# Performance work log

Hardware: AMD Instinct MI355X
Metric: run time of the kernel (lower is better)

The kernel has to match this reference:

```python
import jax, jax.numpy as jnp
import numpy as np

D_MODEL = 2048
NUM_HEADS = 16
HEAD_DIM = D_MODEL // NUM_HEADS
SCALE = 1.0 / np.sqrt(HEAD_DIM).astype(np.float32)
NEG_INF = -1e9


def setup_inputs() -> dict:
    key = jax.random.key(0)
    ks = jax.random.split(key, 10)
    B, S = 2, 2048
    x = jax.random.normal(ks[0], (B, S, D_MODEL), dtype=jnp.float32)
    # causal lower-triangular mask, broadcastable over (B, H)
    causal_mask = jnp.tril(jnp.ones((S, S), dtype=jnp.int32))[None, None]
    init = 1.0 / np.sqrt(D_MODEL)
    def lin(kw, kb):
        W = jax.random.uniform(kw, (D_MODEL, D_MODEL), jnp.float32, -init, init)
        b = jax.random.uniform(kb, (D_MODEL,), jnp.float32, -init, init)
        return W, b
    Wq, bq = lin(ks[1], ks[2])
    Wk, bk = lin(ks[3], ks[4])
    Wv, bv = lin(ks[5], ks[6])
    Wo, bo = lin(ks[7], ks[8])
    return {"x": x, "causal_mask": causal_mask,
            "Wq": Wq, "bq": bq, "Wk": Wk, "bk": bk,
            "Wv": Wv, "bv": bv, "Wo": Wo, "bo": bo}


def reference(x, causal_mask, Wq, bq, Wk, bk, Wv, bv, Wo, bo):
    B, S, _ = x.shape
    def proj(W, b):
        # torch Linear: x @ W.T + b -> (B, H, S, Dh)
        y = jnp.einsum('bsd,ed->bse', x, W) + b
        return y.reshape(B, S, NUM_HEADS, HEAD_DIM).transpose(0, 2, 1, 3)
    q = proj(Wq, bq)
    k = proj(Wk, bk)
    v = proj(Wv, bv)
    # apply_rope is a no-op stub in the source; q, k unchanged.
    scores = jnp.einsum('bhqd,bhkd->bhqk', q, k) * SCALE
    scores = jnp.where(causal_mask == 0, NEG_INF, scores)
    attn = jax.nn.softmax(scores, axis=-1)
    out = jnp.einsum('bhqk,bhkd->bhqd', attn, v)
    out = out.transpose(0, 2, 1, 3).reshape(B, S, D_MODEL)
    return jnp.einsum('bsd,ed->bse', out, Wo) + bo
```

## Files before the change

kernel.cpp:

```cpp
#include <hip/hip_runtime.h>
#include <hip/hip_bf16.h>
#include <stdint.h>
#include <stddef.h>

typedef __bf16 bf16_t;
typedef __bf16 bf16x4_t __attribute__((ext_vector_type(4)));
typedef __bf16 bf16x8_t __attribute__((ext_vector_type(8)));
typedef float f32x4 __attribute__((ext_vector_type(4)));

#define D_MODEL 2048
#define NHEADS 16
#define HDIM 128
#define SEQ 2048
#define BATCH 2
#define MTOT (BATCH * SEQ)
#define SCALE_F 0.08838834764831845f

#define AS1 __attribute__((address_space(1)))
#define AS3 __attribute__((address_space(3)))

__device__ __forceinline__ void load_lds16(const bf16_t* g, bf16_t* l) {
  __builtin_amdgcn_global_load_lds((AS1 void*)(g), (AS3 void*)(l), 16, 0, 0);
}

__global__ void cast_kernel(const float* __restrict__ src, bf16_t* __restrict__ dst, int n4) {
  int i = blockIdx.x * blockDim.x + threadIdx.x;
  if (i < n4) {
    float4 v = ((const float4*)src)[i];
    bf16x4_t o;
    o.x = (bf16_t)v.x; o.y = (bf16_t)v.y; o.z = (bf16_t)v.z; o.w = (bf16_t)v.w;
    ((bf16x4_t*)dst)[i] = o;
  }
}

__global__ __launch_bounds__(256) void gemm_fused(
    const bf16_t* __restrict__ A, const bf16_t* __restrict__ Bm, int mode,
    const float* __restrict__ bias0, const float* __restrict__ bias1,
    const float* __restrict__ bias2,
    bf16_t* __restrict__ Qo, bf16_t* __restrict__ Ko, bf16_t* __restrict__ Vto,
    float* __restrict__ Out) {
  const int K = 2048;
  __shared__ __align__(16) bf16_t lA[128 * 32];
  __shared__ __align__(16) bf16_t lB[128 * 32];
  const int m0 = blockIdx.x * 128;
  const int n0 = blockIdx.y * 128;
  const int t = threadIdx.x;
  const int w = t >> 6, lane = t & 63;
  const int wm = w & 1, wn = w >> 1;
  const int la = lane & 15, lb = lane >> 4;

  f32x4 acc[4][4];
  f32x4 zero = {0.f, 0.f, 0.f, 0.f};
#pragma unroll
  for (int i = 0; i < 4; i++)
#pragma unroll
    for (int j = 0; j < 4; j++) acc[i][j] = zero;

  const bf16_t* gA0 = A + (size_t)(m0 + (t >> 2)) * K + (t & 3) * 8;
  const bf16_t* gA1 = gA0 + (size_t)64 * K;
  const bf16_t* gB0 = Bm + (size_t)(n0 + (t >> 2)) * K + (t & 3) * 8;
  const bf16_t* gB1 = gB0 + (size_t)64 * K;
  bf16_t* sA = lA + t * 8;
  bf16_t* sB = lB + t * 8;

  for (int k0 = 0; k0 < K; k0 += 32) {
    __syncthreads();
    load_lds16(gA0 + k0, sA);
    load_lds16(gA1 + k0, sA + 2048);
    load_lds16(gB0 + k0, sB);
    load_lds16(gB1 + k0, sB + 2048);
    __syncthreads();
    bf16x8_t af[4], bfr[4];
#pragma unroll
    for (int mt = 0; mt < 4; mt++)
      af[mt] = *(const bf16x8_t*)(lA + (wm * 64 + mt * 16 + la) * 32 + lb * 8);
#pragma unroll
    for (int nt = 0; nt < 4; nt++)
      bfr[nt] = *(const bf16x8_t*)(lB + (wn * 64 + nt * 16 + la) * 32 + lb * 8);
#pragma unroll
    for (int mt = 0; mt < 4; mt++)
#pragma unroll
      for (int nt = 0; nt < 4; nt++)
        acc[mt][nt] = __builtin_amdgcn_mfma_f32_16x16x32_bf16(af[mt], bfr[nt], acc[mt][nt], 0, 0, 0);
  }

  if (mode == 0) {
#pragma unroll
    for (int mt = 0; mt < 4; mt++) {
#pragma unroll
      for (int nt = 0; nt < 4; nt++) {
        int m = m0 + wm * 64 + mt * 16 + lb * 4;
        int n = n0 + wn * 64 + nt * 16 + la;
        int b = m >> 11, s = m & 2047;
        int which = n >> 11, hd = n & 2047;
        int h = hd >> 7, d = hd & 127;
        float bv = (which == 0 ? bias0 : which == 1 ? bias1 : bias2)[hd];
        f32x4 v = acc[mt][nt];
        if (which == 2) {
          bf16_t* dst = Vto + ((size_t)(b * NHEADS + h) * HDIM + d) * SEQ + s;
          bf16x4_t pk;
          pk.x = (bf16_t)(v.x + bv); pk.y = (bf16_t)(v.y + bv);
          pk.z = (bf16_t)(v.z + bv); pk.w = (bf16_t)(v.w + bv);
          *(bf16x4_t*)dst = pk;
        } else {
          bf16_t* dst = (which == 0 ? Qo : Ko) + ((size_t)(b * NHEADS + h) * SEQ + s) * HDIM + d;
          dst[0]        = (bf16_t)(v.x + bv);
          dst[HDIM]     = (bf16_t)(v.y + bv);
          dst[2 * HDIM] = (bf16_t)(v.z + bv);
          dst[3 * HDIM] = (bf16_t)(v.w + bv);
        }
      }
    }
  } else {
#pragma unroll
    for (int mt = 0; mt < 4; mt++) {
#pragma unroll
      for (int nt = 0; nt < 4; nt++) {
        int m = m0 + wm * 64 + mt * 16 + lb * 4;
        int n = n0 + wn * 64 + nt * 16 + la;
        float bv = bias0[n];
        f32x4 v = acc[mt][nt];
        float* dst = Out + (size_t)m * D_MODEL + n;
        dst[0]           = v.x + bv;
        dst[D_MODEL]     = v.y + bv;
        dst[2 * D_MODEL] = v.z + bv;
        dst[3 * D_MODEL] = v.w + bv;
      }
    }
  }
}

__global__ __launch_bounds__(256) void flash_attn(
    const bf16_t* __restrict__ Q, const bf16_t* __restrict__ Kg,
    const bf16_t* __restrict__ Vt, bf16_t* __restrict__ O) {
  __shared__ __align__(16) bf16_t lK[64 * 128];
  __shared__ __align__(16) bf16_t lV[128 * 64];
  __shared__ __align__(16) bf16_t lP[128 * 72];
  int g = blockIdx.x;
  int qt, bh;
  if (g < 256) { qt = g >> 5; bh = g & 31; }
  else         { qt = 15 - ((g - 256) >> 5); bh = g & 31; }
  const int q0 = qt * 128;
  const int t = threadIdx.x;
  const int w = t >> 6, lane = t & 63;
  const int la = lane & 15, lb = lane >> 4;

  const bf16_t* Qb = Q + (size_t)bh * SEQ * HDIM;
  const bf16_t* Kb = Kg + (size_t)bh * SEQ * HDIM;
  const bf16_t* Vb = Vt + (size_t)bh * HDIM * SEQ;

  bf16x8_t qf[2][4];
#pragma unroll
  for (int mt = 0; mt < 2; mt++)
#pragma unroll
    for (int ks = 0; ks < 4; ks++)
      qf[mt][ks] = *(const bf16x8_t*)(Qb + (size_t)(q0 + w * 32 + mt * 16 + la) * HDIM + ks * 32 + lb * 8);

  f32x4 oacc[2][8];
  float mrow[2][4], lrow[2][4];
  f32x4 zero = {0.f, 0.f, 0.f, 0.f};
#pragma unroll
  for (int mt = 0; mt < 2; mt++) {
#pragma unroll
    for (int dt = 0; dt < 8; dt++) oacc[mt][dt] = zero;
#pragma unroll
    for (int r = 0; r < 4; r++) { mrow[mt][r] = -3.0e38f; lrow[mt][r] = 0.f; }
  }

  const int nkt = qt * 2 + 2;
  for (int kt = 0; kt < nkt; kt++) {
    const int j0 = kt * 64;
    __syncthreads();
#pragma unroll
    for (int i = 0; i < 4; i++) {
      int slot = t + 256 * i;
      int j = slot >> 4, cc = slot & 15;
      load_lds16(Kb + (size_t)(j0 + j) * HDIM + ((cc ^ (j & 15)) * 8), lK + slot * 8);
    }
#pragma unroll
    for (int i = 0; i < 4; i++) {
      int slot = t + 256 * i;
      int d = slot >> 3, jc = slot & 7;
      load_lds16(Vb + (size_t)d * SEQ + j0 + ((jc ^ (d & 7)) * 8), lV + slot * 8);
    }
    __syncthreads();

    f32x4 sacc[2][4];
#pragma unroll
    for (int mt = 0; mt < 2; mt++)
#pragma unroll
      for (int nt = 0; nt < 4; nt++) sacc[mt][nt] = zero;
#pragma unroll
    for (int ks = 0; ks < 4; ks++) {
#pragma unroll
      for (int nt = 0; nt < 4; nt++) {
        int j = nt * 16 + la;
        int cc = (lb + 4 * ks) ^ (j & 15);
        bf16x8_t kf = *(const bf16x8_t*)(lK + j * 128 + cc * 8);
#pragma unroll
        for (int mt = 0; mt < 2; mt++)
          sacc[mt][nt] = __builtin_amdgcn_mfma_f32_16x16x32_bf16(qf[mt][ks], kf, sacc[mt][nt], 0, 0, 0);
      }
    }

#pragma unroll
    for (int mt = 0; mt < 2; mt++) {
      int qrow = q0 + w * 32 + mt * 16 + lb * 4;
      f32x4 rmax;
#pragma unroll
      for (int r = 0; r < 4; r++) {
        float x = -3.0e38f;
#pragma unroll
        for (int nt = 0; nt < 4; nt++) {
          int j = j0 + nt * 16 + la;
          float sv = sacc[mt][nt][r] * SCALE_F;
          if (j > qrow + r) sv = -3.0e38f;
          sacc[mt][nt][r] = sv;
          x = fmaxf(x, sv);
        }
        rmax[r] = x;
      }
#pragma unroll
      for (int off = 1; off < 16; off <<= 1)
#pragma unroll
        for (int r = 0; r < 4; r++) rmax[r] = fmaxf(rmax[r], __shfl_xor(rmax[r], off));
      f32x4 rsum;
#pragma unroll
      for (int r = 0; r < 4; r++) {
        float mnew = fmaxf(mrow[mt][r], rmax[r]);
        float alpha = __expf(mrow[mt][r] - mnew);
        mrow[mt][r] = mnew;
        lrow[mt][r] *= alpha;
#pragma unroll
        for (int dt = 0; dt < 8; dt++) oacc[mt][dt][r] *= alpha;
        float s = 0.f;
#pragma unroll
        for (int nt = 0; nt < 4; nt++) {
          float pex = __expf(sacc[mt][nt][r] - mnew);
          sacc[mt][nt][r] = pex;
          s += pex;
        }
        rsum[r] = s;
      }
#pragma unroll
      for (int off = 1; off < 16; off <<= 1)
#pragma unroll
        for (int r = 0; r < 4; r++) rsum[r] += __shfl_xor(rsum[r], off);
#pragma unroll
      for (int r = 0; r < 4; r++) lrow[mt][r] += rsum[r];
#pragma unroll
      for (int nt = 0; nt < 4; nt++)
#pragma unroll
        for (int r = 0; r < 4; r++)
          lP[(w * 32 + mt * 16 + lb * 4 + r) * 72 + nt * 16 + la] = (bf16_t)sacc[mt][nt][r];
    }

    bf16x8_t pf[2][2];
#pragma unroll
    for (int mt = 0; mt < 2; mt++)
#pragma unroll
      for (int ks = 0; ks < 2; ks++)
        pf[mt][ks] = *(const bf16x8_t*)(lP + (w * 32 + mt * 16 + la) * 72 + ks * 32 + lb * 8);
#pragma unroll
    for (int ks = 0; ks < 2; ks++) {
#pragma unroll
      for (int dt = 0; dt < 8; dt++) {
        int d = dt * 16 + la;
        int jc = (lb + 4 * ks) ^ (d & 7);
        bf16x8_t vf = *(const bf16x8_t*)(lV + d * 64 + jc * 8);
#pragma unroll
        for (int mt = 0; mt < 2; mt++)
          oacc[mt][dt] = __builtin_amdgcn_mfma_f32_16x16x32_bf16(pf[mt][ks], vf, oacc[mt][dt], 0, 0, 0);
      }
    }
  }

  const int b = bh >> 4, h = bh & 15;
#pragma unroll
  for (int mt = 0; mt < 2; mt++) {
    f32x4 inv;
#pragma unroll
    for (int r = 0; r < 4; r++) inv[r] = 1.0f / lrow[mt][r];
#pragma unroll
    for (int dt = 0; dt < 8; dt++) {
#pragma unroll
      for (int r = 0; r < 4; r++) {
        int q = q0 + w * 32 + mt * 16 + lb * 4 + r;
        int d = h * HDIM + dt * 16 + la;
        O[((size_t)b * SEQ + q) * D_MODEL + d] = (bf16_t)(oacc[mt][dt][r] * inv[r]);
      }
    }
  }
}

extern "C" void kernel_launch(void* const* d_in, const int* in_sizes, int n_in,
                              void* d_out, int out_size, void* d_ws, size_t ws_size,
                              hipStream_t stream) {
  (void)in_sizes; (void)n_in; (void)out_size; (void)ws_size;
  const float* x  = (const float*)d_in[0];
  const float* Wq = (const float*)d_in[2];
  const float* bq = (const float*)d_in[3];
  const float* Wk = (const float*)d_in[4];
  const float* bk = (const float*)d_in[5];
  const float* Wv = (const float*)d_in[6];
  const float* bv = (const float*)d_in[7];
  const float* Wo = (const float*)d_in[8];
  const float* bo = (const float*)d_in[9];
  float* out = (float*)d_out;

  const size_t NBF = (size_t)MTOT * D_MODEL * sizeof(bf16_t);
  const size_t WBF = (size_t)D_MODEL * D_MODEL * sizeof(bf16_t);
  char* p = (char*)d_ws;
  bf16_t* xb   = (bf16_t*)p; p += NBF;
  bf16_t* Wcat = (bf16_t*)p; p += 3 * WBF;
  bf16_t* Wob  = (bf16_t*)p; p += WBF;
  bf16_t* Qb   = (bf16_t*)p; p += NBF;
  bf16_t* Kb   = (bf16_t*)p; p += NBF;
  bf16_t* Vtb  = (bf16_t*)p; p += NBF;
  bf16_t* Ob   = xb;

  const int WN4 = D_MODEL * D_MODEL / 4;
  const int XN4 = MTOT * D_MODEL / 4;
  cast_kernel<<<XN4 / 256, 256, 0, stream>>>(x, xb, XN4);
  cast_kernel<<<WN4 / 256, 256, 0, stream>>>(Wq, Wcat, WN4);
  cast_kernel<<<WN4 / 256, 256, 0, stream>>>(Wk, Wcat + (size_t)D_MODEL * D_MODEL, WN4);
  cast_kernel<<<WN4 / 256, 256, 0, stream>>>(Wv, Wcat + (size_t)2 * D_MODEL * D_MODEL, WN4);
  cast_kernel<<<WN4 / 256, 256, 0, stream>>>(Wo, Wob, WN4);

  gemm_fused<<<dim3(MTOT / 128, 6144 / 128), 256, 0, stream>>>(
      xb, Wcat, 0, bq, bk, bv, Qb, Kb, Vtb, nullptr);

  flash_attn<<<dim3(512), 256, 0, stream>>>(Qb, Kb, Vtb, Ob);

  gemm_fused<<<dim3(MTOT / 128, D_MODEL / 128), 256, 0, stream>>>(
      Ob, Wob, 1, bo, nullptr, nullptr, nullptr, nullptr, nullptr, out);
}
```

Baseline: 448.5 us.

## Double GEMM K-tile with XOR-swizzled LDS, merge weight casts, use exp2 softmax

The GEMM's K step grows from 32 to 64 and the LDS tile layout gets an XOR swizzle, which halves the number of barrier-separated iterations and is meant to avoid LDS bank conflicts on the fragment reads. The four weight cast launches are merged into one 2D-grid launch. Flash attention folds log2(e) into the score scale and uses exp2f in place of __expf. The larger tile doubles the GEMM's LDS footprint, which may lower occupancy.

After: 415.7 us. 1.08x faster.

```diff
diff --git a/kernel.cpp b/kernel.cpp
--- a/kernel.cpp
+++ b/kernel.cpp
@@ -15,6 +15,7 @@
 #define BATCH 2
 #define MTOT (BATCH * SEQ)
 #define SCALE_F 0.08838834764831845f
+#define LOG2E 1.4426950408889634f
 
 #define AS1 __attribute__((address_space(1)))
 #define AS3 __attribute__((address_space(3)))
@@ -33,6 +34,20 @@
   }
 }
 
+__global__ void cast4_kernel(const float* __restrict__ s0, const float* __restrict__ s1,
+                             const float* __restrict__ s2, const float* __restrict__ s3,
+                             bf16_t* __restrict__ dst, int n4) {
+  int i = blockIdx.x * blockDim.x + threadIdx.x;
+  int y = blockIdx.y;
+  if (i < n4) {
+    const float* src = (y == 0) ? s0 : (y == 1) ? s1 : (y == 2) ? s2 : s3;
+    float4 v = ((const float4*)src)[i];
+    bf16x4_t o;
+    o.x = (bf16_t)v.x; o.y = (bf16_t)v.y; o.z = (bf16_t)v.z; o.w = (bf16_t)v.w;
+    ((bf16x4_t*)(dst + (size_t)y * D_MODEL * D_MODEL / 4 * 4))[i] = o;
+  }
+}
+
 __global__ __launch_bounds__(256) void gemm_fused(
     const bf16_t* __restrict__ A, const bf16_t* __restrict__ Bm, int mode,
     const float* __restrict__ bias0, const float* __restrict__ bias1,
@@ -40,8 +55,8 @@
     bf16_t* __restrict__ Qo, bf16_t* __restrict__ Ko, bf16_t* __restrict__ Vto,
     float* __restrict__ Out) {
   const int K = 2048;
-  __shared__ __align__(16) bf16_t lA[128 * 32];
-  __shared__ __align__(16) bf16_t lB[128 * 32];
+  __shared__ __align__(16) bf16_t lA[128 * 64];
+  __shared__ __align__(16) bf16_t lB[128 * 64];
   const int m0 = blockIdx.x * 128;
   const int n0 = blockIdx.y * 128;
   const int t = threadIdx.x;
@@ -56,32 +71,41 @@
 #pragma unroll
     for (int j = 0; j < 4; j++) acc[i][j] = zero;
 
-  const bf16_t* gA0 = A + (size_t)(m0 + (t >> 2)) * K + (t & 3) * 8;
-  const bf16_t* gA1 = gA0 + (size_t)64 * K;
-  const bf16_t* gB0 = Bm + (size_t)(n0 + (t >> 2)) * K + (t & 3) * 8;
-  const bf16_t* gB1 = gB0 + (size_t)64 * K;
+  const int row0 = t >> 3, cc = t & 7;
+  const int ccs = cc ^ (row0 & 7);
+  const bf16_t* gA = A + (size_t)(m0 + row0) * K + ccs * 8;
+  const bf16_t* gB = Bm + (size_t)(n0 + row0) * K + ccs * 8;
   bf16_t* sA = lA + t * 8;
   bf16_t* sB = lB + t * 8;
 
-  for (int k0 = 0; k0 < K; k0 += 32) {
+  for (int k0 = 0; k0 < K; k0 += 64) {
     __syncthreads();
-    load_lds16(gA0 + k0, sA);
-    load_lds16(gA1 + k0, sA + 2048);
-    load_lds16(gB0 + k0, sB);
-    load_lds16(gB1 + k0, sB + 2048);
+#pragma unroll
+    for (int i = 0; i < 4; i++)
+      load_lds16(gA + k0 + (size_t)(32 * i) * K, sA + 2048 * i);
+#pragma unroll
+    for (int i = 0; i < 4; i++)
+      load_lds16(gB + k0 + (size_t)(32 * i) * K, sB + 2048 * i);
     __syncthreads();
-    bf16x8_t af[4], bfr[4];
-#pragma unroll
-    for (int mt = 0; mt < 4; mt++)
-      af[mt] = *(const bf16x8_t*)(lA + (wm * 64 + mt * 16 + la) * 32 + lb * 8);
-#pragma unroll
-    for (int nt = 0; nt < 4; nt++)
-      bfr[nt] = *(const bf16x8_t*)(lB + (wn * 64 + nt * 16 + la) * 32 + lb * 8);
-#pragma unroll
-    for (int mt = 0; mt < 4; mt++)
-#pragma unroll
-      for (int nt = 0; nt < 4; nt++)
-        acc[mt][nt] = __builtin_amdgcn_mfma_f32_16x16x32_bf16(af[mt], bfr[nt], acc[mt][nt], 0, 0, 0);
+#pragma unroll
+    for (int ks = 0; ks < 2; ks++) {
+      bf16x8_t af[4], bfr[4];
+#pragma unroll
+      for (int mt = 0; mt < 4; mt++) {
+        int row = wm * 64 + mt * 16 + la;
+        af[mt] = *(const bf16x8_t*)(lA + row * 64 + (((ks * 4 + lb) ^ (la & 7)) * 8));
+      }
+#pragma unroll
+      for (int nt = 0; nt < 4; nt++) {
+        int row = wn * 64 + nt * 16 + la;
+        bfr[nt] = *(const bf16x8_t*)(lB + row * 64 + (((ks * 4 + lb) ^ (la & 7)) * 8));
+      }
+#pragma unroll
+      for (int mt = 0; mt < 4; mt++)
+#pragma unroll
+        for (int nt = 0; nt < 4; nt++)
+          acc[mt][nt] = __builtin_amdgcn_mfma_f32_16x16x32_bf16(af[mt], bfr[nt], acc[mt][nt], 0, 0, 0);
+    }
   }
 
   if (mode == 0) {
@@ -167,6 +191,7 @@
     for (int r = 0; r < 4; r++) { mrow[mt][r] = -3.0e38f; lrow[mt][r] = 0.f; }
   }
 
+  const float scale2 = SCALE_F * LOG2E;
   const int nkt = qt * 2 + 2;
   for (int kt = 0; kt < nkt; kt++) {
     const int j0 = kt * 64;
@@ -213,7 +238,7 @@
 #pragma unroll
         for (int nt = 0; nt < 4; nt++) {
           int j = j0 + nt * 16 + la;
-          float sv = sacc[mt][nt][r] * SCALE_F;
+          float sv = sacc[mt][nt][r] * scale2;
           if (j > qrow + r) sv = -3.0e38f;
           sacc[mt][nt][r] = sv;
           x = fmaxf(x, sv);
@@ -228,7 +253,7 @@
 #pragma unroll
       for (int r = 0; r < 4; r++) {
         float mnew = fmaxf(mrow[mt][r], rmax[r]);
-        float alpha = __expf(mrow[mt][r] - mnew);
+        float alpha = exp2f(mrow[mt][r] - mnew);
         mrow[mt][r] = mnew;
         lrow[mt][r] *= alpha;
 #pragma unroll
@@ -236,7 +261,7 @@
         float s = 0.f;
 #pragma unroll
         for (int nt = 0; nt < 4; nt++) {
-          float pex = __expf(sacc[mt][nt][r] - mnew);
+          float pex = exp2f(sacc[mt][nt][r] - mnew);
           sacc[mt][nt][r] = pex;
           s += pex;
         }
@@ -312,20 +337,17 @@
   const size_t WBF = (size_t)D_MODEL * D_MODEL * sizeof(bf16_t);
   char* p = (char*)d_ws;
   bf16_t* xb   = (bf16_t*)p; p += NBF;
-  bf16_t* Wcat = (bf16_t*)p; p += 3 * WBF;
-  bf16_t* Wob  = (bf16_t*)p; p += WBF;
+  bf16_t* Wcat = (bf16_t*)p; p += 4 * WBF;
   bf16_t* Qb   = (bf16_t*)p; p += NBF;
   bf16_t* Kb   = (bf16_t*)p; p += NBF;
   bf16_t* Vtb  = (bf16_t*)p; p += NBF;
+  bf16_t* Wob  = Wcat + (size_t)3 * D_MODEL * D_MODEL;
   bf16_t* Ob   = xb;
 
   const int WN4 = D_MODEL * D_MODEL / 4;
   const int XN4 = MTOT * D_MODEL / 4;
   cast_kernel<<<XN4 / 256, 256, 0, stream>>>(x, xb, XN4);
-  cast_kernel<<<WN4 / 256, 256, 0, stream>>>(Wq, Wcat, WN4);
-  cast_kernel<<<WN4 / 256, 256, 0, stream>>>(Wk, Wcat + (size_t)D_MODEL * D_MODEL, WN4);
-  cast_kernel<<<WN4 / 256, 256, 0, stream>>>(Wv, Wcat + (size_t)2 * D_MODEL * D_MODEL, WN4);
-  cast_kernel<<<WN4 / 256, 256, 0, stream>>>(Wo, Wob, WN4);
+  cast4_kernel<<<dim3(WN4 / 256, 4), 256, 0, stream>>>(Wq, Wk, Wv, Wo, Wcat, WN4);
 
   gemm_fused<<<dim3(MTOT / 128, 6144 / 128), 256, 0, stream>>>(
       xb, Wcat, 0, bq, bk, bv, Qb, Kb, Vtb, nullptr);
```
